# Kernel optimization log

Measured on AMD Instinct MI355X. Metric: run time of the kernel, lower is better.

Reference implementation:

```python
import jax, jax.numpy as jnp
import numpy as np

N, E, G, H = 4096, 8192, 64, 128  # nodes, edges, graphs, hidden dim
NODE_DIM, EDGE_DIM = 11, 5


def _linear_params(key, fan_in, fan_out):
    kw, kb = jax.random.split(key)
    s = 1.0 / np.sqrt(fan_in)
    w = jax.random.uniform(kw, (fan_in, fan_out), minval=-s, maxval=s, dtype=jnp.float32)
    b = jax.random.uniform(kb, (fan_out,), minval=-s, maxval=s, dtype=jnp.float32)
    return w, b


def setup_inputs() -> dict:
    key = jax.random.key(0)
    ks = jax.random.split(key, 10)
    x = jax.random.normal(ks[0], (N, NODE_DIM), dtype=jnp.float32)
    edge_attr = jax.random.normal(ks[1], (E, EDGE_DIM), dtype=jnp.float32)
    edge_index = jax.random.randint(ks[2], (2, E), 0, N, dtype=jnp.int64)
    batch = jnp.sort(jax.random.randint(ks[3], (N,), 0, G, dtype=jnp.int64))
    # preprocess MLP: node_dim -> 128 -> 128
    p1_w, p1_b = _linear_params(ks[4], NODE_DIM, H)
    p2_w, p2_b = _linear_params(ks[5], H, H)
    # edge net: edge_dim -> 128 -> 256 -> 128 -> 128*128 (ReLU between, none after last)
    e1_w, e1_b = _linear_params(ks[6], EDGE_DIM, 128)
    e2_w, e2_b = _linear_params(ks[7], 128, 256)
    e3_w, e3_b = _linear_params(ks[8], 256, 128)
    e4_w, e4_b = _linear_params(ks[9], 128, H * H)
    return {"x": x, "edge_attr": edge_attr, "edge_index": edge_index, "batch": batch,
            "p1_w": p1_w, "p1_b": p1_b, "p2_w": p2_w, "p2_b": p2_b,
            "e1_w": e1_w, "e1_b": e1_b, "e2_w": e2_w, "e2_b": e2_b,
            "e3_w": e3_w, "e3_b": e3_b, "e4_w": e4_w, "e4_b": e4_b}


def reference(x, edge_attr, edge_index, batch,
              p1_w, p1_b, p2_w, p2_b,
              e1_w, e1_b, e2_w, e2_b, e3_w, e3_b, e4_w, e4_b):
    # node preprocess MLP (maps 11-dim features to 128 so NNConv dims are consistent)
    h = jax.nn.relu(x @ p1_w + p1_b) @ p2_w + p2_b  # [N, H]
    # edge network -> per-edge weight matrix [E, H, H]
    e = jax.nn.relu(edge_attr @ e1_w + e1_b)
    e = jax.nn.relu(e @ e2_w + e2_b)
    e = jax.nn.relu(e @ e3_w + e3_b)
    W = (e @ e4_w + e4_b).reshape(E, H, H)
    # NNConv (root_weight=False, bias=False, aggr='mean'):
    src, dst = edge_index[0], edge_index[1]
    msg = jnp.einsum('ei,eio->eo', h[src], W)  # gather + per-edge matmul, [E, H]
    agg = jax.ops.segment_sum(msg, dst, num_segments=N)
    cnt = jax.ops.segment_sum(jnp.ones((E,), msg.dtype), dst, num_segments=N)
    h_out = agg / jnp.maximum(cnt, 1.0)[:, None]  # scatter-mean, [N, H]
    # global add pool over graphs
    pooled = jax.ops.segment_sum(h_out, batch, num_segments=G)  # [G, H]
    return pooled
```

## Files before the change

### kernel.cpp

```cpp
#include <hip/hip_runtime.h>
#include <stdint.h>
#include <stddef.h>

typedef unsigned short ushort_t;
typedef __attribute__((ext_vector_type(8))) short short8;
typedef __attribute__((ext_vector_type(4))) short short4v;
typedef __attribute__((ext_vector_type(4))) float f32x4;
typedef __attribute__((ext_vector_type(4))) unsigned int uint4v;

#define GL2LDS(gsrc, ldst) \
  __builtin_amdgcn_global_load_lds((const __attribute__((address_space(1))) void*)(gsrc), \
                                   (__attribute__((address_space(3))) void*)(ldst), 16, 0, 0)

__device__ __forceinline__ float bf2f(ushort_t u) {
  union { unsigned int i; float f; } v; v.i = ((unsigned int)u) << 16; return v.f;
}
__device__ __forceinline__ ushort_t f2bf(float f) {
  unsigned int u = __builtin_bit_cast(unsigned int, f);
  unsigned int r = (u + 0x7fffu + ((u >> 16) & 1u)) >> 16;
  return (ushort_t)r;
}

__global__ void k_front(const float* __restrict__ e4w, const float* __restrict__ e4b,
                        ushort_t* __restrict__ e4wT,
                        const float* __restrict__ e2w, ushort_t* __restrict__ w2h,
                        ushort_t* __restrict__ w2l,
                        const float* __restrict__ e3w, ushort_t* __restrict__ w3h,
                        ushort_t* __restrict__ w3l,
                        const float* __restrict__ x, const float* __restrict__ p1w,
                        const float* __restrict__ p1b, const float* __restrict__ p2w,
                        const float* __restrict__ p2b, ushort_t* __restrict__ h_node) {
  __shared__ char smem[128 * 65 * 4];
  int bid = blockIdx.x, tid = threadIdx.x;

  if (bid < 258) {
    float (*t)[65] = (float(*)[65])smem;
    int c0 = bid * 64;
    for (int it = 0; it < 32; ++it) {
      int idx = it * 256 + tid;
      int cc = idx >> 7, oo = idx & 127;
      int c = c0 + cc;
      float v = (c < 16384) ? e4w[(size_t)c * 128 + oo] : e4b[(size_t)(c - 16384) * 128 + oo];
      t[oo][cc] = v;
    }
    __syncthreads();
    for (int it = 0; it < 32; ++it) {
      int idx = it * 256 + tid;
      int oo = idx >> 6, cc = idx & 63;
      e4wT[(size_t)oo * 16512 + c0 + cc] = f2bf(t[oo][cc]);
    }
  } else if (bid < 514) {
    const float* in;
    ushort_t *oh, *ol;
    int lg2n, K, id0;
    if (bid < 386) { in = e2w; oh = w2h; ol = w2l; K = 128; lg2n = 8; id0 = (bid - 258) * 256; }
    else           { in = e3w; oh = w3h; ol = w3l; K = 256; lg2n = 7; id0 = (bid - 386) * 256; }
    int id = id0 + tid;
    int N = 1 << lg2n;
    int k = id >> lg2n, o = id & (N - 1);
    float v = in[id];
    ushort_t hb = f2bf(v);
    float lo = v - bf2f(hb);
    oh[(size_t)o * K + k] = hb;
    ol[(size_t)o * K + k] = f2bf(lo);
  } else {
    float (*xs)[12] = (float(*)[12])smem;
    float (*t1)[128] = (float(*)[128])(smem + 8 * 12 * 4);
    int n0 = (bid - 514) * 8;
    if (tid < 88) { int n = tid / 11, j = tid % 11; xs[n][j] = x[(size_t)(n0 + n) * 11 + j]; }
    __syncthreads();
    for (int it = 0; it < 4; ++it) {
      int p = it * 256 + tid;
      int n = p >> 7, o = p & 127;
      float a = p1b[o];
#pragma unroll
      for (int j = 0; j < 11; ++j) a += xs[n][j] * p1w[j * 128 + o];
      t1[n][o] = fmaxf(a, 0.f);
    }
    __syncthreads();
    {
      int o = tid & 127, nb = tid >> 7;
      float a0 = p2b[o], a1_ = a0, a2_ = a0, a3_ = a0;
      for (int k4 = 0; k4 < 32; ++k4) {
        float w0 = p2w[(k4 * 4 + 0) * 128 + o];
        float w1 = p2w[(k4 * 4 + 1) * 128 + o];
        float w2 = p2w[(k4 * 4 + 2) * 128 + o];
        float w3 = p2w[(k4 * 4 + 3) * 128 + o];
        float4 v0 = *(const float4*)&t1[nb + 0][k4 * 4];
        float4 v1 = *(const float4*)&t1[nb + 2][k4 * 4];
        float4 v2 = *(const float4*)&t1[nb + 4][k4 * 4];
        float4 v3 = *(const float4*)&t1[nb + 6][k4 * 4];
        a0 += v0.x * w0 + v0.y * w1 + v0.z * w2 + v0.w * w3;
        a1_ += v1.x * w0 + v1.y * w1 + v1.z * w2 + v1.w * w3;
        a2_ += v2.x * w0 + v2.y * w1 + v2.z * w2 + v2.w * w3;
        a3_ += v3.x * w0 + v3.y * w1 + v3.z * w2 + v3.w * w3;
      }
      h_node[(size_t)(n0 + nb + 0) * 128 + o] = f2bf(a0);
      h_node[(size_t)(n0 + nb + 2) * 128 + o] = f2bf(a1_);
      h_node[(size_t)(n0 + nb + 4) * 128 + o] = f2bf(a2_);
      h_node[(size_t)(n0 + nb + 6) * 128 + o] = f2bf(a3_);
    }
  }
}

__global__ void k_mlp(const float* __restrict__ ea, const int* __restrict__ eidx,
                      const ushort_t* __restrict__ h_node,
                      const float* __restrict__ e1w, const float* __restrict__ e1b,
                      const ushort_t* __restrict__ w2h, const ushort_t* __restrict__ w2l,
                      const float* __restrict__ e2b,
                      const ushort_t* __restrict__ w3h, const ushort_t* __restrict__ w3l,
                      const float* __restrict__ e3b,
                      float* __restrict__ e3Tf, ushort_t* __restrict__ h_src) {
  __shared__ float eas[32][6];
  __shared__ int srcs[32];
  __shared__ ushort_t a1h[32 * 136], a1l[32 * 136];
  __shared__ ushort_t a2h[32 * 264], a2l[32 * 264];
  __shared__ float a3t[128 * 40];

  int tid = threadIdx.x;
  int w = tid >> 6, ln = tid & 63, g = ln >> 4, l15 = ln & 15;
  int e0 = blockIdx.x * 32;

  if (tid < 160) { int n = tid / 5, j = tid % 5; eas[n][j] = ea[(size_t)(e0 + n) * 5 + j]; }
  if (tid < 32) srcs[tid] = eidx[e0 + tid];
  __syncthreads();

  {
    int n = tid >> 4, oc = (tid & 15) * 8;
    *(short8*)(h_src + (size_t)(e0 + n) * 128 + oc) =
        *(const short8*)(h_node + (size_t)srcs[n] * 128 + oc);
  }

  {
    int n = tid >> 4, ob = (tid & 15) * 8;
    float acc1[8];
    float4 ba = *(const float4*)(e1b + ob);
    float4 bb = *(const float4*)(e1b + ob + 4);
    acc1[0] = ba.x; acc1[1] = ba.y; acc1[2] = ba.z; acc1[3] = ba.w;
    acc1[4] = bb.x; acc1[5] = bb.y; acc1[6] = bb.z; acc1[7] = bb.w;
#pragma unroll
    for (int j = 0; j < 5; ++j) {
      float aj = eas[n][j];
      float4 wa = *(const float4*)(e1w + j * 128 + ob);
      float4 wb = *(const float4*)(e1w + j * 128 + ob + 4);
      acc1[0] = fmaf(aj, wa.x, acc1[0]); acc1[1] = fmaf(aj, wa.y, acc1[1]);
      acc1[2] = fmaf(aj, wa.z, acc1[2]); acc1[3] = fmaf(aj, wa.w, acc1[3]);
      acc1[4] = fmaf(aj, wb.x, acc1[4]); acc1[5] = fmaf(aj, wb.y, acc1[5]);
      acc1[6] = fmaf(aj, wb.z, acc1[6]); acc1[7] = fmaf(aj, wb.w, acc1[7]);
    }
    short8 ph, pl;
#pragma unroll
    for (int q = 0; q < 8; ++q) {
      float v = fmaxf(acc1[q], 0.f);
      ushort_t hb = f2bf(v);
      ph[q] = (short)hb;
      pl[q] = (short)f2bf(v - bf2f(hb));
    }
    int addr = n * 136 + ob;
    *(short8*)(a1h + addr) = ph;
    *(short8*)(a1l + addr) = pl;
  }
  __syncthreads();

  {
    int cbase = w * 32;
    f32x4 acc2[2][2];
#pragma unroll
    for (int rf = 0; rf < 2; ++rf)
#pragma unroll
      for (int cf = 0; cf < 2; ++cf) acc2[rf][cf] = (f32x4){0.f, 0.f, 0.f, 0.f};
    short8 ah[2][4], al[2][4];
#pragma unroll
    for (int rf = 0; rf < 2; ++rf)
#pragma unroll
      for (int ks = 0; ks < 4; ++ks) {
        int row = rf * 16 + l15;
        int addr = row * 136 + (ks * 4 + g) * 8;
        ah[rf][ks] = *(const short8*)(a1h + addr);
        al[rf][ks] = *(const short8*)(a1l + addr);
      }
#pragma unroll
    for (int ks = 0; ks < 4; ++ks) {
#pragma unroll
      for (int cf = 0; cf < 2; ++cf) {
        int nrow = cbase + cf * 16 + l15;
        size_t boff = (size_t)nrow * 128 + (ks * 4 + g) * 8;
        short8 bh = *(const short8*)(w2h + boff);
        short8 bl = *(const short8*)(w2l + boff);
#pragma unroll
        for (int rf = 0; rf < 2; ++rf) {
          acc2[rf][cf] = __builtin_amdgcn_mfma_f32_16x16x32_bf16(ah[rf][ks], bh, acc2[rf][cf], 0, 0, 0);
          acc2[rf][cf] = __builtin_amdgcn_mfma_f32_16x16x32_bf16(al[rf][ks], bh, acc2[rf][cf], 0, 0, 0);
          acc2[rf][cf] = __builtin_amdgcn_mfma_f32_16x16x32_bf16(ah[rf][ks], bl, acc2[rf][cf], 0, 0, 0);
        }
      }
    }
#pragma unroll
    for (int rf = 0; rf < 2; ++rf)
#pragma unroll
      for (int cf = 0; cf < 2; ++cf) {
        int col = cbase + cf * 16 + l15;
        float b = e2b[col];
#pragma unroll
        for (int r2 = 0; r2 < 4; ++r2) {
          int row = rf * 16 + g * 4 + r2;
          float v = fmaxf(acc2[rf][cf][r2] + b, 0.f);
          ushort_t hb = f2bf(v);
          int addr = row * 264 + col;
          a2h[addr] = hb;
          a2l[addr] = f2bf(v - bf2f(hb));
        }
      }
  }
  __syncthreads();

  {
    f32x4 acc3[2];
    acc3[0] = (f32x4){0.f, 0.f, 0.f, 0.f};
    acc3[1] = (f32x4){0.f, 0.f, 0.f, 0.f};
    int nrow = w * 16 + l15;
#pragma unroll
    for (int ks = 0; ks < 8; ++ks) {
      short8 a2hf[2], a2lf[2];
#pragma unroll
      for (int rf = 0; rf < 2; ++rf) {
        int row = rf * 16 + l15;
        int addr = row * 264 + (ks * 4 + g) * 8;
        a2hf[rf] = *(const short8*)(a2h + addr);
        a2lf[rf] = *(const short8*)(a2l + addr);
      }
      size_t boff = (size_t)nrow * 256 + (ks * 4 + g) * 8;
      short8 bh = *(const short8*)(w3h + boff);
      short8 bl = *(const short8*)(w3l + boff);
#pragma unroll
      for (int rf = 0; rf < 2; ++rf) {
        acc3[rf] = __builtin_amdgcn_mfma_f32_16x16x32_bf16(a2hf[rf], bh, acc3[rf], 0, 0, 0);
        acc3[rf] = __builtin_amdgcn_mfma_f32_16x16x32_bf16(a2lf[rf], bh, acc3[rf], 0, 0, 0);
        acc3[rf] = __builtin_amdgcn_mfma_f32_16x16x32_bf16(a2hf[rf], bl, acc3[rf], 0, 0, 0);
      }
    }
    int col = w * 16 + l15;
    float b = e3b[col];
#pragma unroll
    for (int rf = 0; rf < 2; ++rf)
#pragma unroll
      for (int r2 = 0; r2 < 4; ++r2) {
        int row = rf * 16 + g * 4 + r2;
        float v = fmaxf(acc3[rf][r2] + b, 0.f);
        a3t[col * 40 + row] = v;
      }
  }
  __syncthreads();

  {
    int o = tid >> 2, eq = (tid & 3) * 8;
    float4 q0 = *(const float4*)(a3t + o * 40 + eq);
    float4 q1 = *(const float4*)(a3t + o * 40 + eq + 4);
    *(float4*)(e3Tf + (size_t)o * 8192 + e0 + eq) = q0;
    *(float4*)(e3Tf + (size_t)o * 8192 + e0 + eq + 4) = q1;
  }
}

__launch_bounds__(512, 1)
__global__ void k_gemm(const ushort_t* __restrict__ h_src, const float* __restrict__ e3Tf,
                       const ushort_t* __restrict__ e4wT, ushort_t* __restrict__ partial) {
  __shared__ ushort_t bufA[16384];
  __shared__ float e3s[32 * 128];

  int tid = threadIdx.x;
  int w = tid >> 6, ln = tid & 63;
  int g = ln >> 4, l15 = ln & 15;
  int bid = blockIdx.x;
  int mt = bid >> 2, s = bid & 3;
  int e0 = mt * 128;
  int t0 = s * 32;
  int nt = (s == 3) ? 33 : 32;

  {
    const ushort_t* hbase = h_src + (size_t)e0 * 128;
#pragma unroll
    for (int it = 0; it < 4; ++it) {
      int chunk = it * 512 + tid;
      int r = chunk >> 4;
      int Gt = (chunk & 15) ^ (r & 15);
      GL2LDS(hbase + r * 128 + Gt * 8, (char*)&bufA[0] + (it * 512 + w * 64) * 16);
    }
#pragma unroll
    for (int it = 0; it < 2; ++it) {
      int chunk = it * 512 + tid;
      int tl = chunk >> 5, cc = chunk & 31;
      GL2LDS(e3Tf + (size_t)(t0 + tl) * 8192 + e0 + cc * 4,
             (char*)&e3s[0] + (it * 512 + w * 64) * 16);
    }
  }
  asm volatile("s_waitcnt vmcnt(0)" ::: "memory");
  __builtin_amdgcn_s_barrier();
  asm volatile("" ::: "memory");

  short8 afr[8][4];
#pragma unroll
  for (int rf = 0; rf < 8; ++rf)
#pragma unroll
    for (int ks = 0; ks < 4; ++ks) {
      int row = rf * 16 + l15;
      int gr = (ks * 4 + g) ^ (row & 15);
      afr[rf][ks] = *(const short8*)((const char*)&bufA[0] + row * 256 + gr * 16);
    }

  f32x4 acc[8];
#pragma unroll
  for (int rf = 0; rf < 8; ++rf) acc[rf] = (f32x4){0.f, 0.f, 0.f, 0.f};

  const f32x4 zero4 = {0.f, 0.f, 0.f, 0.f};
  int nrow = w * 16 + l15;

  const ushort_t* brow = e4wT + (size_t)nrow * 16512 + (size_t)t0 * 128;
  short8 bcur[4], bnxt[4];
#pragma unroll
  for (int ks = 0; ks < 4; ++ks) bcur[ks] = *(const short8*)(brow + (ks * 4 + g) * 8);
  brow += 128;

  for (int tl = 0; tl < nt; ++tl) {
    int tg = t0 + tl;

    if (tl + 1 < nt) {
#pragma unroll
      for (int ks = 0; ks < 4; ++ks) bnxt[ks] = *(const short8*)(brow + (ks * 4 + g) * 8);
      brow += 128;
    }

    f32x4 part[8];
#pragma unroll
    for (int rf = 0; rf < 8; ++rf)
      part[rf] = __builtin_amdgcn_mfma_f32_16x16x32_bf16(afr[rf][0], bcur[0], zero4, 0, 0, 0);
#pragma unroll
    for (int ks = 1; ks < 4; ++ks)
#pragma unroll
      for (int rf = 0; rf < 8; ++rf)
        part[rf] = __builtin_amdgcn_mfma_f32_16x16x32_bf16(afr[rf][ks], bcur[ks], part[rf], 0, 0, 0);

    if (tg < 128) {
#pragma unroll
      for (int rf = 0; rf < 8; ++rf) {
        float4 ev = *(const float4*)&e3s[tl * 128 + rf * 16 + g * 4];
        acc[rf][0] = fmaf(ev.x, part[rf][0], acc[rf][0]);
        acc[rf][1] = fmaf(ev.y, part[rf][1], acc[rf][1]);
        acc[rf][2] = fmaf(ev.z, part[rf][2], acc[rf][2]);
        acc[rf][3] = fmaf(ev.w, part[rf][3], acc[rf][3]);
      }
    } else {
#pragma unroll
      for (int rf = 0; rf < 8; ++rf)
#pragma unroll
        for (int r2 = 0; r2 < 4; ++r2) acc[rf][r2] += part[rf][r2];
    }

    if (tl + 1 < nt) {
#pragma unroll
      for (int ks = 0; ks < 4; ++ks) bcur[ks] = bnxt[ks];
    }
  }

#pragma unroll
  for (int rf = 0; rf < 8; ++rf)
#pragma unroll
    for (int r2 = 0; r2 < 4; ++r2) {
      int row = rf * 16 + g * 4 + r2;
      partial[((size_t)s * 8192 + e0 + row) * 128 + nrow] = f2bf(acc[rf][r2]);
    }
}

__global__ void k_reduce(const ushort_t* __restrict__ partial, const int* __restrict__ eidx,
                         float* __restrict__ agg, float* __restrict__ cnt) {
  int id = blockIdx.x * 256 + threadIdx.x;
  int e = id >> 4, oc = (id & 15) * 8;
  float v[8];
#pragma unroll
  for (int q = 0; q < 8; ++q) v[q] = 0.f;
#pragma unroll
  for (int s2 = 0; s2 < 4; ++s2) {
    short8 p = *(const short8*)(partial + ((size_t)s2 * 8192 + e) * 128 + oc);
#pragma unroll
    for (int q = 0; q < 8; ++q) v[q] += bf2f((ushort_t)p[q]);
  }
  int d = eidx[8192 + e];
  float* dst = agg + (size_t)d * 128 + oc;
#pragma unroll
  for (int q = 0; q < 8; ++q) atomicAdd(dst + q, v[q]);
  if ((id & 15) == 0) atomicAdd(&cnt[d], 1.0f);
}

__device__ __forceinline__ int lbound(const int* a, int n, int v) {
  int lo = 0, hi = n;
  while (lo < hi) { int m = (lo + hi) >> 1; if (a[m] < v) lo = m + 1; else hi = m; }
  return lo;
}

__global__ void k_pool(const float* __restrict__ agg, const float* __restrict__ cnt,
                       const int* __restrict__ batch, float* __restrict__ out) {
  int gph = blockIdx.x, o = threadIdx.x;
  int lo = lbound(batch, 4096, gph);
  int hi = lbound(batch, 4096, gph + 1);
  float a = 0.f;
  for (int n = lo; n < hi; ++n) a += agg[(size_t)n * 128 + o] / fmaxf(cnt[n], 1.0f);
  out[(size_t)gph * 128 + o] = a;
}

extern "C" void kernel_launch(void* const* d_in, const int* in_sizes, int n_in,
                              void* d_out, int out_size, void* d_ws, size_t ws_size,
                              hipStream_t stream) {
  (void)in_sizes; (void)n_in; (void)out_size; (void)ws_size;
  const float* x   = (const float*)d_in[0];
  const float* ea  = (const float*)d_in[1];
  const int*   ei  = (const int*)d_in[2];
  const int*   bat = (const int*)d_in[3];
  const float* p1w = (const float*)d_in[4];  const float* p1b = (const float*)d_in[5];
  const float* p2w = (const float*)d_in[6];  const float* p2b = (const float*)d_in[7];
  const float* e1w = (const float*)d_in[8];  const float* e1b = (const float*)d_in[9];
  const float* e2w = (const float*)d_in[10]; const float* e2b = (const float*)d_in[11];
  const float* e3w = (const float*)d_in[12]; const float* e3b = (const float*)d_in[13];
  const float* e4w = (const float*)d_in[14]; const float* e4b = (const float*)d_in[15];

  char* ws = (char*)d_ws;
  ushort_t* e4wT   = (ushort_t*)(ws + 0);
  ushort_t* h_node = (ushort_t*)(ws + 4227072);
  ushort_t* h_srcp = (ushort_t*)(ws + 5275648);
  float*    e3Tf   = (float*)(ws + 7372800);
  ushort_t* part   = (ushort_t*)(ws + 11567104);
  float*    agg    = (float*)(ws + 19955712);
  float*    cnt    = (float*)(ws + 22052864);
  ushort_t* w2h    = (ushort_t*)(ws + 22069248);
  ushort_t* w2l    = (ushort_t*)(ws + 22134784);
  ushort_t* w3h    = (ushort_t*)(ws + 22200320);
  ushort_t* w3l    = (ushort_t*)(ws + 22265856);

  hipMemsetAsync(ws + 19955712, 0, 2097152 + 16384, stream);

  k_front <<<1026, 256, 0, stream>>>(e4w, e4b, e4wT, e2w, w2h, w2l, e3w, w3h, w3l,
                                     x, p1w, p1b, p2w, p2b, h_node);
  k_mlp   <<<256,  512, 0, stream>>>(ea, ei, h_node, e1w, e1b, w2h, w2l, e2b,
                                     w3h, w3l, e3b, e3Tf, h_srcp);
  k_gemm  <<<256,  512, 0, stream>>>(h_srcp, e3Tf, e4wT, part);
  k_reduce<<<512,  256, 0, stream>>>(part, ei, agg, cnt);
  k_pool  <<<64,   128, 0, stream>>>(agg, cnt, bat, (float*)d_out);
}
```

Baseline: 208.1 us.

## Gather source node features directly in GEMM and prepack MLP weights in fragment order

```diff
diff --git a/kernel.cpp b/kernel.cpp
--- a/kernel.cpp
+++ b/kernel.cpp
@@ -6,7 +6,6 @@
 typedef __attribute__((ext_vector_type(8))) short short8;
 typedef __attribute__((ext_vector_type(4))) short short4v;
 typedef __attribute__((ext_vector_type(4))) float f32x4;
-typedef __attribute__((ext_vector_type(4))) unsigned int uint4v;
 
 #define GL2LDS(gsrc, ldst) \
   __builtin_amdgcn_global_load_lds((const __attribute__((address_space(1))) void*)(gsrc), \
@@ -49,24 +48,40 @@
       int oo = idx >> 6, cc = idx & 63;
       e4wT[(size_t)oo * 16512 + c0 + cc] = f2bf(t[oo][cc]);
     }
-  } else if (bid < 514) {
-    const float* in;
-    ushort_t *oh, *ol;
-    int lg2n, K, id0;
-    if (bid < 386) { in = e2w; oh = w2h; ol = w2l; K = 128; lg2n = 8; id0 = (bid - 258) * 256; }
-    else           { in = e3w; oh = w3h; ol = w3l; K = 256; lg2n = 7; id0 = (bid - 386) * 256; }
-    int id = id0 + tid;
-    int N = 1 << lg2n;
-    int k = id >> lg2n, o = id & (N - 1);
-    float v = in[id];
-    ushort_t hb = f2bf(v);
-    float lo = v - bf2f(hb);
-    oh[(size_t)o * K + k] = hb;
-    ol[(size_t)o * K + k] = f2bf(lo);
+  } else if (bid < 274) {
+    int id = (bid - 258) * 256 + tid;
+    int cf = id >> 8, ks = (id >> 6) & 3, ln = id & 63;
+    int n = cf * 16 + (ln & 15);
+    int k0 = (ks * 4 + (ln >> 4)) * 8;
+    short8 ph, pl;
+#pragma unroll
+    for (int q = 0; q < 8; ++q) {
+      float v = e2w[(size_t)(k0 + q) * 256 + n];
+      ushort_t hb = f2bf(v);
+      ph[q] = (short)hb;
+      pl[q] = (short)f2bf(v - bf2f(hb));
+    }
+    *(short8*)(w2h + (size_t)id * 8) = ph;
+    *(short8*)(w2l + (size_t)id * 8) = pl;
+  } else if (bid < 290) {
+    int id = (bid - 274) * 256 + tid;
+    int cf = id >> 9, ks = (id >> 6) & 7, ln = id & 63;
+    int n = cf * 16 + (ln & 15);
+    int k0 = (ks * 4 + (ln >> 4)) * 8;
+    short8 ph, pl;
+#pragma unroll
+    for (int q = 0; q < 8; ++q) {
+      float v = e3w[(size_t)(k0 + q) * 128 + n];
+      ushort_t hb = f2bf(v);
+      ph[q] = (short)hb;
+      pl[q] = (short)f2bf(v - bf2f(hb));
+    }
+    *(short8*)(w3h + (size_t)id * 8) = ph;
+    *(short8*)(w3l + (size_t)id * 8) = pl;
   } else {
     float (*xs)[12] = (float(*)[12])smem;
     float (*t1)[128] = (float(*)[128])(smem + 8 * 12 * 4);
-    int n0 = (bid - 514) * 8;
+    int n0 = (bid - 290) * 8;
     if (tid < 88) { int n = tid / 11, j = tid % 11; xs[n][j] = x[(size_t)(n0 + n) * 11 + j]; }
     __syncthreads();
     for (int it = 0; it < 4; ++it) {
@@ -103,16 +118,14 @@
   }
 }
 
-__global__ void k_mlp(const float* __restrict__ ea, const int* __restrict__ eidx,
-                      const ushort_t* __restrict__ h_node,
+__global__ void k_mlp(const float* __restrict__ ea,
                       const float* __restrict__ e1w, const float* __restrict__ e1b,
                       const ushort_t* __restrict__ w2h, const ushort_t* __restrict__ w2l,
                       const float* __restrict__ e2b,
                       const ushort_t* __restrict__ w3h, const ushort_t* __restrict__ w3l,
                       const float* __restrict__ e3b,
-                      float* __restrict__ e3Tf, ushort_t* __restrict__ h_src) {
+                      float* __restrict__ e3Tf) {
   __shared__ float eas[32][6];
-  __shared__ int srcs[32];
   __shared__ ushort_t a1h[32 * 136], a1l[32 * 136];
   __shared__ ushort_t a2h[32 * 264], a2l[32 * 264];
   __shared__ float a3t[128 * 40];
@@ -122,14 +135,7 @@
   int e0 = blockIdx.x * 32;
 
   if (tid < 160) { int n = tid / 5, j = tid % 5; eas[n][j] = ea[(size_t)(e0 + n) * 5 + j]; }
-  if (tid < 32) srcs[tid] = eidx[e0 + tid];
   __syncthreads();
-
-  {
-    int n = tid >> 4, oc = (tid & 15) * 8;
-    *(short8*)(h_src + (size_t)(e0 + n) * 128 + oc) =
-        *(const short8*)(h_node + (size_t)srcs[n] * 128 + oc);
-  }
 
   {
     int n = tid >> 4, ob = (tid & 15) * 8;
@@ -163,7 +169,6 @@
   __syncthreads();
 
   {
-    int cbase = w * 32;
     f32x4 acc2[2][2];
 #pragma unroll
     for (int rf = 0; rf < 2; ++rf)
@@ -182,29 +187,29 @@
 #pragma unroll
     for (int ks = 0; ks < 4; ++ks) {
 #pragma unroll
-      for (int cf = 0; cf < 2; ++cf) {
-        int nrow = cbase + cf * 16 + l15;
-        size_t boff = (size_t)nrow * 128 + (ks * 4 + g) * 8;
-        short8 bh = *(const short8*)(w2h + boff);
-        short8 bl = *(const short8*)(w2l + boff);
+      for (int cfi = 0; cfi < 2; ++cfi) {
+        int cf = w * 2 + cfi;
+        size_t poff = (size_t)(((cf * 4 + ks) << 6) + ln) * 8;
+        short8 bh = *(const short8*)(w2h + poff);
+        short8 bl = *(const short8*)(w2l + poff);
 #pragma unroll
         for (int rf = 0; rf < 2; ++rf) {
-          acc2[rf][cf] = __builtin_amdgcn_mfma_f32_16x16x32_bf16(ah[rf][ks], bh, acc2[rf][cf], 0, 0, 0);
-          acc2[rf][cf] = __builtin_amdgcn_mfma_f32_16x16x32_bf16(al[rf][ks], bh, acc2[rf][cf], 0, 0, 0);
-          acc2[rf][cf] = __builtin_amdgcn_mfma_f32_16x16x32_bf16(ah[rf][ks], bl, acc2[rf][cf], 0, 0, 0);
+          acc2[rf][cfi] = __builtin_amdgcn_mfma_f32_16x16x32_bf16(ah[rf][ks], bh, acc2[rf][cfi], 0, 0, 0);
+          acc2[rf][cfi] = __builtin_amdgcn_mfma_f32_16x16x32_bf16(al[rf][ks], bh, acc2[rf][cfi], 0, 0, 0);
+          acc2[rf][cfi] = __builtin_amdgcn_mfma_f32_16x16x32_bf16(ah[rf][ks], bl, acc2[rf][cfi], 0, 0, 0);
         }
       }
     }
 #pragma unroll
     for (int rf = 0; rf < 2; ++rf)
 #pragma unroll
-      for (int cf = 0; cf < 2; ++cf) {
-        int col = cbase + cf * 16 + l15;
+      for (int cfi = 0; cfi < 2; ++cfi) {
+        int col = (w * 2 + cfi) * 16 + l15;
         float b = e2b[col];
 #pragma unroll
         for (int r2 = 0; r2 < 4; ++r2) {
           int row = rf * 16 + g * 4 + r2;
-          float v = fmaxf(acc2[rf][cf][r2] + b, 0.f);
+          float v = fmaxf(acc2[rf][cfi][r2] + b, 0.f);
           ushort_t hb = f2bf(v);
           int addr = row * 264 + col;
           a2h[addr] = hb;
@@ -218,7 +223,6 @@
     f32x4 acc3[2];
     acc3[0] = (f32x4){0.f, 0.f, 0.f, 0.f};
     acc3[1] = (f32x4){0.f, 0.f, 0.f, 0.f};
-    int nrow = w * 16 + l15;
 #pragma unroll
     for (int ks = 0; ks < 8; ++ks) {
       short8 a2hf[2], a2lf[2];
@@ -229,9 +233,9 @@
         a2hf[rf] = *(const short8*)(a2h + addr);
         a2lf[rf] = *(const short8*)(a2l + addr);
       }
-      size_t boff = (size_t)nrow * 256 + (ks * 4 + g) * 8;
-      short8 bh = *(const short8*)(w3h + boff);
-      short8 bl = *(const short8*)(w3l + boff);
+      size_t poff = (size_t)(((w * 8 + ks) << 6) + ln) * 8;
+      short8 bh = *(const short8*)(w3h + poff);
+      short8 bl = *(const short8*)(w3l + poff);
 #pragma unroll
       for (int rf = 0; rf < 2; ++rf) {
         acc3[rf] = __builtin_amdgcn_mfma_f32_16x16x32_bf16(a2hf[rf], bh, acc3[rf], 0, 0, 0);
@@ -262,7 +266,8 @@
 }
 
 __launch_bounds__(512, 1)
-__global__ void k_gemm(const ushort_t* __restrict__ h_src, const float* __restrict__ e3Tf,
+__global__ void k_gemm(const ushort_t* __restrict__ h_node, const int* __restrict__ eidx,
+                       const float* __restrict__ e3Tf,
                        const ushort_t* __restrict__ e4wT, ushort_t* __restrict__ partial) {
   __shared__ ushort_t bufA[16384];
   __shared__ float e3s[32 * 128];
@@ -277,13 +282,13 @@
   int nt = (s == 3) ? 33 : 32;
 
   {
-    const ushort_t* hbase = h_src + (size_t)e0 * 128;
 #pragma unroll
     for (int it = 0; it < 4; ++it) {
       int chunk = it * 512 + tid;
       int r = chunk >> 4;
       int Gt = (chunk & 15) ^ (r & 15);
-      GL2LDS(hbase + r * 128 + Gt * 8, (char*)&bufA[0] + (it * 512 + w * 64) * 16);
+      int se = eidx[e0 + r];
+      GL2LDS(h_node + (size_t)se * 128 + Gt * 8, (char*)&bufA[0] + (it * 512 + w * 64) * 16);
     }
 #pragma unroll
     for (int it = 0; it < 2; ++it) {
@@ -424,23 +429,22 @@
   char* ws = (char*)d_ws;
   ushort_t* e4wT   = (ushort_t*)(ws + 0);
   ushort_t* h_node = (ushort_t*)(ws + 4227072);
-  ushort_t* h_srcp = (ushort_t*)(ws + 5275648);
-  float*    e3Tf   = (float*)(ws + 7372800);
-  ushort_t* part   = (ushort_t*)(ws + 11567104);
-  float*    agg    = (float*)(ws + 19955712);
-  float*    cnt    = (float*)(ws + 22052864);
-  ushort_t* w2h    = (ushort_t*)(ws + 22069248);
-  ushort_t* w2l    = (ushort_t*)(ws + 22134784);
-  ushort_t* w3h    = (ushort_t*)(ws + 22200320);
-  ushort_t* w3l    = (ushort_t*)(ws + 22265856);
-
-  hipMemsetAsync(ws + 19955712, 0, 2097152 + 16384, stream);
-
-  k_front <<<1026, 256, 0, stream>>>(e4w, e4b, e4wT, e2w, w2h, w2l, e3w, w3h, w3l,
+  float*    e3Tf   = (float*)(ws + 5275648);
+  ushort_t* part   = (ushort_t*)(ws + 9469952);
+  float*    agg    = (float*)(ws + 17858560);
+  float*    cnt    = (float*)(ws + 19955712);
+  ushort_t* w2h    = (ushort_t*)(ws + 19972096);
+  ushort_t* w2l    = (ushort_t*)(ws + 20037632);
+  ushort_t* w3h    = (ushort_t*)(ws + 20103168);
+  ushort_t* w3l    = (ushort_t*)(ws + 20168704);
+
+  hipMemsetAsync(ws + 17858560, 0, 2097152 + 16384, stream);
+
+  k_front <<<802,  256, 0, stream>>>(e4w, e4b, e4wT, e2w, w2h, w2l, e3w, w3h, w3l,
                                      x, p1w, p1b, p2w, p2b, h_node);
-  k_mlp   <<<256,  512, 0, stream>>>(ea, ei, h_node, e1w, e1b, w2h, w2l, e2b,
-                                     w3h, w3l, e3b, e3Tf, h_srcp);
-  k_gemm  <<<256,  512, 0, stream>>>(h_srcp, e3Tf, e4wT, part);
+  k_mlp   <<<256,  512, 0, stream>>>(ea, e1w, e1b, w2h, w2l, e2b,
+                                     w3h, w3l, e3b, e3Tf);
+  k_gemm  <<<256,  512, 0, stream>>>(h_node, ei, e3Tf, e4wT, part);
   k_reduce<<<512,  256, 0, stream>>>(part, ei, agg, cnt);
   k_pool  <<<64,   128, 0, stream>>>(agg, cnt, bat, (float*)d_out);
 }
```

After: 204.5 us. No clear change (-1.7%).
